# Kernel tuning notes

Hardware: AMD Instinct MI355X
Metric: run time of the kernel (lower is better)

The kernel has to match this reference:

```python
import jax, jax.numpy as jnp
import numpy as np

B, S, H = 2, 2048, 2048
HQ, HKV, DK, DV = 32, 8, 64, 64
G = HQ // HKV  # queries per kv group
SCALE = 1.0 / DK ** 0.5


def setup_inputs() -> dict:
    key = jax.random.key(0)
    k1, k2, k3, k4 = jax.random.split(key, 4)
    qkv_out = HQ * DK + HKV * (DK + DV)
    x = jax.random.normal(k1, (B, S, H), dtype=jnp.float32)
    Wqkv = jax.random.normal(k2, (H, qkv_out), dtype=jnp.float32) * (1.0 / np.sqrt(H))
    Wout = jax.random.normal(k3, (HQ * DV, H), dtype=jnp.float32) * (1.0 / np.sqrt(HQ * DV))
    b_out = jax.random.normal(k4, (H,), dtype=jnp.float32) * 0.01
    # causal mask [B, 1, S, S]; mask==0 positions are disallowed
    mask = jnp.broadcast_to(jnp.tril(jnp.ones((S, S), dtype=jnp.int32)), (B, 1, S, S))
    return {"x": x, "Wqkv": Wqkv, "Wout": Wout, "b_out": b_out, "mask": mask}


def reference(x, Wqkv, Wout, b_out, mask):
    # fused QKV projection (bias=False)
    qkv = x @ Wqkv  # [B, S, HQ*DK + HKV*(DK+DV)]
    tq, tk = HQ * DK, HKV * DK
    Q = qkv[..., :tq].reshape(B, S, HKV, G, DK)          # [B,S,n,g,d]
    K = qkv[..., tq:tq + tk].reshape(B, S, HKV, DK)       # [B,S,n,d]
    V = qkv[..., tq + tk:].reshape(B, S, HKV, DV)         # [B,S,n,e]
    # scores: [B, n(kv heads), g(group), s(query), t(key)]
    scores = jnp.einsum('bsngd,btnd->bngst', Q, K) * SCALE
    # mask [B,1,S,S] -> broadcast over n,g as [B,1,1,S,S]
    m = mask[:, :, None, :, :]
    scores = jnp.where(m == 0, -jnp.inf, scores)
    probs = jax.nn.softmax(scores, axis=-1)  # dropout p=0 -> identity
    attn = jnp.einsum('bngst,btne->bsnge', probs, V)      # [B,S,n,g,e]
    out = attn.reshape(B, S, HQ * DV) @ Wout + b_out       # [B,S,H]
    return out
```

## Files before the change

### kernel.cpp

```cpp
#include <hip/hip_runtime.h>

#define SEQ    2048
#define HDIM   2048
#define QKV_LD 3072
#define K_BASE 2048
#define V_BASE 2560
#define ATT_SCALE 0.125f
#define SM_MAX 20.0f
#define QK_MUL 0.18033688f
#define ZINIT  -28.8539008f

typedef __bf16 bf16x8 __attribute__((ext_vector_type(8)));
typedef float  f32x4  __attribute__((ext_vector_type(4)));
typedef float  f32x16 __attribute__((ext_vector_type(16)));
typedef unsigned short u16x8 __attribute__((ext_vector_type(8)));
typedef unsigned       u32x4 __attribute__((ext_vector_type(4)));

__device__ __forceinline__ void async_copy16(void* lds, const void* g) {
  __builtin_amdgcn_global_load_lds(
      (const __attribute__((address_space(1))) unsigned*)g,
      (__attribute__((address_space(3))) unsigned*)lds, 16, 0, 0);
}

__device__ __forceinline__ unsigned cvtpk(float lo, float hi) {
  unsigned r;
  asm("v_cvt_pk_bf16_f32 %0, %1, %2" : "=v"(r) : "v"(lo), "v"(hi));
  return r;
}
__device__ __forceinline__ void pl32swap(unsigned& a, unsigned& b) {
  asm("v_permlane32_swap_b32 %0, %1" : "+v"(a), "+v"(b));
}

__global__ void detect_dtype(const unsigned* __restrict__ p0,
                             const unsigned* __restrict__ p1,
                             const unsigned* __restrict__ p2,
                             const unsigned* __restrict__ p3,
                             int* __restrict__ flags) {
  const unsigned* ptrs[4] = {p0, p1, p2, p3};
  const int lane = threadIdx.x;
#pragma unroll
  for (int i = 0; i < 4; ++i) {
    int cnt = 0;
#pragma unroll
    for (int j = 0; j < 8; ++j) {
      unsigned w = ptrs[i][lane * 8 + j];
      unsigned e = (w >> 7) & 0xFF;
      cnt += (e >= 90 && e <= 160) ? 1 : 0;
    }
    for (int off = 32; off; off >>= 1) cnt += __shfl_down(cnt, off);
    if (lane == 0) flags[i] = (cnt < 350) ? 1 : 0;
  }
  if (lane == 0) flags[4] = 0;
}

__global__ __launch_bounds__(256) void cast_f32_bf16(const float* __restrict__ s,
                                                     __bf16* __restrict__ d) {
  const size_t i = ((size_t)blockIdx.x * 256 + threadIdx.x) * 8;
  float4 a = *(const float4*)(s + i);
  float4 b = *(const float4*)(s + i + 4);
  bf16x8 o;
  o[0] = (__bf16)a.x; o[1] = (__bf16)a.y; o[2] = (__bf16)a.z; o[3] = (__bf16)a.w;
  o[4] = (__bf16)b.x; o[5] = (__bf16)b.y; o[6] = (__bf16)b.z; o[7] = (__bf16)b.w;
  *(bf16x8*)(d + i) = o;
}

__global__ __launch_bounds__(256) void transpose_cast(const float* __restrict__ W,
                                                      __bf16* __restrict__ WT,
                                                      int K, int N) {
  __shared__ float T[64][68];
  const int tid = threadIdx.x;
  const int kb = blockIdx.y * 64, nb = blockIdx.x * 64;
  const int r = tid >> 2, cq = tid & 3;
  const float* src = W + (size_t)(kb + r) * N + nb + cq * 16;
  float4 f0 = ((const float4*)src)[0];
  float4 f1 = ((const float4*)src)[1];
  float4 f2 = ((const float4*)src)[2];
  float4 f3 = ((const float4*)src)[3];
  *(float4*)&T[r][cq * 16 + 0]  = f0;
  *(float4*)&T[r][cq * 16 + 4]  = f1;
  *(float4*)&T[r][cq * 16 + 8]  = f2;
  *(float4*)&T[r][cq * 16 + 12] = f3;
  __syncthreads();
  __bf16* dst = WT + (size_t)(nb + r) * K + kb + cq * 16;
  bf16x8 o0, o1;
#pragma unroll
  for (int j = 0; j < 8; ++j) o0[j] = (__bf16)T[cq * 16 + j][r];
#pragma unroll
  for (int j = 0; j < 8; ++j) o1[j] = (__bf16)T[cq * 16 + 8 + j][r];
  *(bf16x8*)dst = o0;
  *(bf16x8*)(dst + 8) = o1;
}

#define GT_ELE (256 * 64)

template <typename OutT>
__global__ __launch_bounds__(512, 2) void gemm256(const __bf16* __restrict__ A,
                                                  const __bf16* __restrict__ Bt,
                                                  const float* __restrict__ bias,
                                                  OutT* __restrict__ C,
                                                  int M, int N, int K) {
  extern __shared__ __align__(16) __bf16 smem[];
  __bf16* Asm = smem;
  __bf16* Bsm = smem + 2 * GT_ELE;

  const int tid = threadIdx.x;
  const int w = tid >> 6, lane = tid & 63;
  const int lr = lane & 15, lg = lane >> 4;
  const int wm = w >> 2, wn = w & 3;
  const int m0 = blockIdx.y * 256, n0 = blockIdx.x * 256;
  const int KT = K >> 6;

  const int lrow = lane >> 3;
  const int lc8  = ((lane & 7) ^ lrow) * 8;

  f32x4 acc[2][4][2][2];
#pragma unroll
  for (int a = 0; a < 2; ++a)
#pragma unroll
    for (int b = 0; b < 4; ++b)
#pragma unroll
      for (int c = 0; c < 2; ++c)
#pragma unroll
        for (int d = 0; d < 2; ++d) acc[a][b][c][d] = (f32x4){0.f, 0.f, 0.f, 0.f};

  bf16x8 af[4][2], bf[2][2];

  const __bf16* gA = A + (size_t)m0 * K;
  const __bf16* gB = Bt + (size_t)n0 * K;

  auto stA = [&](int h, int t) {
    __bf16* base = Asm + (size_t)(t & 1) * GT_ELE + (h * 128 + 16 * w) * 64;
    const __bf16* s = gA + (size_t)(h * 128 + 16 * w + lrow) * K + (size_t)t * 64 + lc8;
    async_copy16(base, s);
    async_copy16(base + 8 * 64, s + (size_t)8 * K);
  };
  auto stB = [&](int h, int t) {
    __bf16* base = Bsm + (size_t)(t & 1) * GT_ELE + (h * 128 + 16 * w) * 64;
    const __bf16* s = gB + (size_t)(h * 128 + 16 * w + lrow) * K + (size_t)t * 64 + lc8;
    async_copy16(base, s);
    async_copy16(base + 8 * 64, s + (size_t)8 * K);
  };

#define LOAD_A(mq)                                                              \
  {                                                                             \
    _Pragma("unroll") for (int mf = 0; mf < 4; ++mf)                            \
        _Pragma("unroll") for (int kk = 0; kk < 2; ++kk)                        \
            af[mf][kk] = *(const bf16x8*)&Ac[((mq) * 128 + wm * 64 + mf * 16 +  \
                                             lr) * 64 +                         \
                                            (((kk * 4 + lg) ^ (lr & 7)) << 3)]; \
  }
#define LOAD_B(nq)                                                              \
  {                                                                             \
    _Pragma("unroll") for (int nf = 0; nf < 2; ++nf)                            \
        _Pragma("unroll") for (int kk = 0; kk < 2; ++kk)                        \
            bf[nf][kk] = *(const bf16x8*)&Bc[((nq) * 128 + wn * 32 + nf * 16 +  \
                                             lr) * 64 +                         \
                                            (((kk * 4 + lg) ^ (lr & 7)) << 3)]; \
  }
#define MFMA_Q(mq, nq)                                                          \
  {                                                                             \
    __builtin_amdgcn_s_setprio(1);                                              \
    _Pragma("unroll") for (int mf = 0; mf < 4; ++mf)                            \
        _Pragma("unroll") for (int nf = 0; nf < 2; ++nf)                        \
            _Pragma("unroll") for (int kk = 0; kk < 2; ++kk)                    \
                acc[mq][mf][nq][nf] = __builtin_amdgcn_mfma_f32_16x16x32_bf16(  \
                    af[mf][kk], bf[nf][kk], acc[mq][mf][nq][nf], 0, 0, 0);      \
    __builtin_amdgcn_s_setprio(0);                                              \
  }
#define WAIT_LGKM                                                               \
  asm volatile("s_waitcnt lgkmcnt(0)" ::: "memory");                            \
  __builtin_amdgcn_sched_barrier(0);

  stA(0, 0); stB(1, 0); stA(1, 0); stB(0, 0);
  stA(0, 1); stB(1, 1);

  for (int kt = 0; kt < KT; ++kt) {
    const __bf16* Ac = Asm + (size_t)(kt & 1) * GT_ELE;
    const __bf16* Bc = Bsm + (size_t)(kt & 1) * GT_ELE;
    const bool p1 = kt + 1 < KT, p2 = kt + 2 < KT;

    if (p1) stA(1, kt + 1);
    if (p1) asm volatile("s_waitcnt vmcnt(6)" ::: "memory");
    else    asm volatile("s_waitcnt vmcnt(0)" ::: "memory");
    __builtin_amdgcn_s_barrier();
    LOAD_A(0); LOAD_B(0);
    WAIT_LGKM; MFMA_Q(0, 0);
    __builtin_amdgcn_s_barrier();

    LOAD_B(1);
    if (p1) stB(0, kt + 1);
    __builtin_amdgcn_s_barrier();
    WAIT_LGKM; MFMA_Q(0, 1);
    __builtin_amdgcn_s_barrier();

    LOAD_A(1);
    if (p2) stA(0, kt + 2);
    __builtin_amdgcn_s_barrier();
    WAIT_LGKM; MFMA_Q(1, 1);
    __builtin_amdgcn_s_barrier();

    LOAD_B(0);
    if (p2) stB(1, kt + 2);
    __builtin_amdgcn_s_barrier();
    WAIT_LGKM; MFMA_Q(1, 0);
    __builtin_amdgcn_s_barrier();
  }

#pragma unroll
  for (int mq = 0; mq < 2; ++mq)
#pragma unroll
    for (int mf = 0; mf < 4; ++mf)
#pragma unroll
      for (int nq = 0; nq < 2; ++nq)
#pragma unroll
        for (int nf = 0; nf < 2; ++nf)
#pragma unroll
          for (int r = 0; r < 4; ++r) {
            int row = m0 + mq * 128 + wm * 64 + mf * 16 + 4 * lg + r;
            int col = n0 + nq * 128 + wn * 32 + nf * 16 + lr;
            float v = acc[mq][mf][nq][nf][r];
            if (bias) v += bias[col];
            C[(size_t)row * N + col] = (OutT)v;
          }
#undef LOAD_A
#undef LOAD_B
#undef MFMA_Q
#undef WAIT_LGKM
}

#define GA_ELE (256 * 64)
#define GB_ELE (128 * 64)

template <typename OutT>
__global__ __launch_bounds__(512, 2) void gemm256x128(const __bf16* __restrict__ A,
                                                      const __bf16* __restrict__ Bt,
                                                      const float* __restrict__ bias,
                                                      OutT* __restrict__ C,
                                                      int M, int N, int K) {
  extern __shared__ __align__(16) __bf16 smem[];
  __bf16* Asm = smem;
  __bf16* Bsm = smem + 2 * GA_ELE;

  const int tid = threadIdx.x;
  const int w = tid >> 6, lane = tid & 63;
  const int lr = lane & 15, lg = lane >> 4;
  const int wm = w >> 2, wn = w & 3;
  const int m0 = blockIdx.y * 256, n0 = blockIdx.x * 128;
  const int KT = K >> 6;

  const int lrow = lane >> 3;
  const int lc8  = ((lane & 7) ^ lrow) * 8;

  f32x4 acc[2][4][2];
#pragma unroll
  for (int a = 0; a < 2; ++a)
#pragma unroll
    for (int b = 0; b < 4; ++b)
#pragma unroll
      for (int c = 0; c < 2; ++c) acc[a][b][c] = (f32x4){0.f, 0.f, 0.f, 0.f};

  bf16x8 af[4][2], bf[2][2];

  const __bf16* gA = A + (size_t)m0 * K;
  const __bf16* gB = Bt + (size_t)n0 * K;

  auto stA = [&](int h, int t) {
    __bf16* base = Asm + (size_t)(t & 1) * GA_ELE + (h * 128 + 16 * w) * 64;
    const __bf16* s = gA + (size_t)(h * 128 + 16 * w + lrow) * K + (size_t)t * 64 + lc8;
    async_copy16(base, s);
    async_copy16(base + 8 * 64, s + (size_t)8 * K);
  };
  auto stB = [&](int t) {
    __bf16* base = Bsm + (size_t)(t & 1) * GB_ELE + (16 * w) * 64;
    const __bf16* s = gB + (size_t)(16 * w + lrow) * K + (size_t)t * 64 + lc8;
    async_copy16(base, s);
    async_copy16(base + 8 * 64, s + (size_t)8 * K);
  };

#define LOAD_A(mq)                                                              \
  {                                                                             \
    _Pragma("unroll") for (int mf = 0; mf < 4; ++mf)                            \
        _Pragma("unroll") for (int kk = 0; kk < 2; ++kk)                        \
            af[mf][kk] = *(const bf16x8*)&Ac[((mq) * 128 + wm * 64 + mf * 16 +  \
                                             lr) * 64 +                         \
                                            (((kk * 4 + lg) ^ (lr & 7)) << 3)]; \
  }
#define LOAD_B                                                                  \
  {                                                                             \
    _Pragma("unroll") for (int nf = 0; nf < 2; ++nf)                            \
        _Pragma("unroll") for (int kk = 0; kk < 2; ++kk)                        \
            bf[nf][kk] = *(const bf16x8*)&Bc[(wn * 32 + nf * 16 + lr) * 64 +    \
                                            (((kk * 4 + lg) ^ (lr & 7)) << 3)]; \
  }
#define MFMA_Q(mq)                                                              \
  {                                                                             \
    __builtin_amdgcn_s_setprio(1);                                              \
    _Pragma("unroll") for (int mf = 0; mf < 4; ++mf)                            \
        _Pragma("unroll") for (int nf = 0; nf < 2; ++nf)                        \
            _Pragma("unroll") for (int kk = 0; kk < 2; ++kk)                    \
                acc[mq][mf][nf] = __builtin_amdgcn_mfma_f32_16x16x32_bf16(      \
                    af[mf][kk], bf[nf][kk], acc[mq][mf][nf], 0, 0, 0);          \
    __builtin_amdgcn_s_setprio(0);                                              \
  }
#define WAIT_LGKM                                                               \
  asm volatile("s_waitcnt lgkmcnt(0)" ::: "memory");                            \
  __builtin_amdgcn_sched_barrier(0);

  stA(0, 0); stB(0); stA(1, 0);
  stA(0, 1); stB(1);

  for (int kt = 0; kt < KT; ++kt) {
    const __bf16* Ac = Asm + (size_t)(kt & 1) * GA_ELE;
    const __bf16* Bc = Bsm + (size_t)(kt & 1) * GB_ELE;
    const bool p1 = kt + 1 < KT, p2 = kt + 2 < KT;

    if (p1) stA(1, kt + 1);
    if (p1) asm volatile("s_waitcnt vmcnt(6)" ::: "memory");
    else    asm volatile("s_waitcnt vmcnt(0)" ::: "memory");
    __builtin_amdgcn_s_barrier();
    LOAD_A(0); LOAD_B;
    WAIT_LGKM; MFMA_Q(0);
    __builtin_amdgcn_s_barrier();

    LOAD_A(1);
    if (p2) { stA(0, kt + 2); stB(kt + 2); }
    __builtin_amdgcn_s_barrier();
    WAIT_LGKM; MFMA_Q(1);
    __builtin_amdgcn_s_barrier();
  }

#pragma unroll
  for (int mq = 0; mq < 2; ++mq)
#pragma unroll
    for (int mf = 0; mf < 4; ++mf)
#pragma unroll
      for (int nf = 0; nf < 2; ++nf)
#pragma unroll
        for (int r = 0; r < 4; ++r) {
          int row = m0 + mq * 128 + wm * 64 + mf * 16 + 4 * lg + r;
          int col = n0 + wn * 32 + nf * 16 + lr;
          float v = acc[mq][mf][nf][r];
          if (bias) v += bias[col];
          C[(size_t)row * N + col] = (OutT)v;
        }
#undef LOAD_A
#undef LOAD_B
#undef MFMA_Q
#undef WAIT_LGKM
}

template <typename OutT>
__global__ __launch_bounds__(256) void gemm128(const __bf16* __restrict__ A,
                                               const __bf16* __restrict__ Bt,
                                               const float* __restrict__ bias,
                                               OutT* __restrict__ C,
                                               int M, int N, int K) {
  __shared__ __bf16 As[128 * 32];
  __shared__ __bf16 Bs[128 * 32];
  const int tid = threadIdx.x;
  const int w = tid >> 6, lane = tid & 63;
  const int lr = lane & 15, lg = lane >> 4;
  const int wm = w >> 1, wn = w & 1;
  const int m0 = blockIdx.y * 128, n0 = blockIdx.x * 128;

  f32x4 acc[4][4];
#pragma unroll
  for (int i = 0; i < 4; ++i)
#pragma unroll
    for (int j = 0; j < 4; ++j) acc[i][j] = (f32x4){0.f, 0.f, 0.f, 0.f};

  const int srow = 32 * w + (lane >> 2);
  const int scol = (lane & 3) * 8;
  const __bf16* ga = A + (size_t)(m0 + srow) * K + scol;
  const __bf16* gb = Bt + (size_t)(n0 + srow) * K + scol;
  __bf16* la0 = &As[(32 * w) * 32];
  __bf16* la1 = &As[(32 * w + 16) * 32];
  __bf16* lb0 = &Bs[(32 * w) * 32];
  __bf16* lb1 = &Bs[(32 * w + 16) * 32];

  for (int k0 = 0; k0 < K; k0 += 32) {
    async_copy16(la0, ga + k0);
    async_copy16(la1, ga + (size_t)16 * K + k0);
    async_copy16(lb0, gb + k0);
    async_copy16(lb1, gb + (size_t)16 * K + k0);
    __syncthreads();
    bf16x8 af[4], bfr[4];
#pragma unroll
    for (int mf = 0; mf < 4; ++mf)
      af[mf] = *(const bf16x8*)&As[(64 * wm + 16 * mf + lr) * 32 + 8 * lg];
#pragma unroll
    for (int nf = 0; nf < 4; ++nf)
      bfr[nf] = *(const bf16x8*)&Bs[(64 * wn + 16 * nf + lr) * 32 + 8 * lg];
#pragma unroll
    for (int mf = 0; mf < 4; ++mf)
#pragma unroll
      for (int nf = 0; nf < 4; ++nf)
        acc[mf][nf] = __builtin_amdgcn_mfma_f32_16x16x32_bf16(af[mf], bfr[nf],
                                                              acc[mf][nf], 0, 0, 0);
    __syncthreads();
  }

#pragma unroll
  for (int mf = 0; mf < 4; ++mf)
#pragma unroll
    for (int nf = 0; nf < 4; ++nf)
#pragma unroll
      for (int r = 0; r < 4; ++r) {
        int row = m0 + 64 * wm + 16 * mf + 4 * lg + r;
        int col = n0 + 64 * wn + 16 * nf + lr;
        float v = acc[mf][nf][r];
        if (bias) v += bias[col];
        C[(size_t)row * N + col] = (OutT)v;
      }
}

template <typename OutT>
__global__ __launch_bounds__(256) void gemm64(const void* __restrict__ Araw,
                                              const void* __restrict__ Braw,
                                              const void* __restrict__ biasraw,
                                              const int* __restrict__ flags,
                                              int fa, int fb, int fbias,
                                              OutT* __restrict__ C,
                                              int M, int N, int K) {
  __shared__ __bf16 As[64][40];
  __shared__ __bf16 Bs[64][40];
  const bool a_f32 = flags[fa] != 0;
  const bool b_f32 = flags[fb] != 0;
  const bool c_f32 = flags[fbias] != 0;
  const int tid = threadIdx.x;
  const int wave = tid >> 6, lane = tid & 63;
  const int lr = lane & 15, lg = lane >> 4;
  const int m0 = blockIdx.y * 64, n0 = blockIdx.x * 64;
  f32x4 acc[4];
#pragma unroll
  for (int i = 0; i < 4; ++i) acc[i] = (f32x4){0.f, 0.f, 0.f, 0.f};
  const int ar = tid >> 2, ac = (tid & 3) * 8;
  const int bn = tid & 63, bk0 = (tid >> 6) * 8;
  for (int k0 = 0; k0 < K; k0 += 32) {
    bf16x8 av;
    if (a_f32) {
      const float* p = (const float*)Araw + (size_t)(m0 + ar) * K + (k0 + ac);
#pragma unroll
      for (int j = 0; j < 8; ++j) av[j] = (__bf16)p[j];
    } else {
      av = *(const bf16x8*)((const __bf16*)Araw + (size_t)(m0 + ar) * K + (k0 + ac));
    }
    *(bf16x8*)&As[ar][ac] = av;
    if (b_f32) {
      const float* p = (const float*)Braw + (size_t)(k0 + bk0) * N + (n0 + bn);
#pragma unroll
      for (int j = 0; j < 8; ++j) Bs[bn][bk0 + j] = (__bf16)p[(size_t)j * N];
    } else {
      const __bf16* p = (const __bf16*)Braw + (size_t)(k0 + bk0) * N + (n0 + bn);
#pragma unroll
      for (int j = 0; j < 8; ++j) Bs[bn][bk0 + j] = p[(size_t)j * N];
    }
    __syncthreads();
    bf16x8 a = *(const bf16x8*)&As[wave * 16 + lr][lg * 8];
#pragma unroll
    for (int nt = 0; nt < 4; ++nt) {
      bf16x8 b = *(const bf16x8*)&Bs[nt * 16 + lr][lg * 8];
      acc[nt] = __builtin_amdgcn_mfma_f32_16x16x32_bf16(a, b, acc[nt], 0, 0, 0);
    }
    __syncthreads();
  }
#pragma unroll
  for (int nt = 0; nt < 4; ++nt)
#pragma unroll
    for (int r = 0; r < 4; ++r) {
      int row = m0 + wave * 16 + lg * 4 + r;
      int col = n0 + nt * 16 + lr;
      float v = acc[nt][r];
      if (biasraw) {
        v += c_f32 ? ((const float*)biasraw)[col]
                   : (float)((const __bf16*)biasraw)[col];
      }
      C[(size_t)row * N + col] = (OutT)v;
    }
}

__global__ __launch_bounds__(256) void attn_fused4(const __bf16* __restrict__ qkv,
                                                   __bf16* __restrict__ attn_out) {
  __shared__ __bf16 Ks[2][64][64];
  __shared__ __bf16 Vt[2][64][72];

  const int tid  = threadIdx.x;
  const int w    = tid >> 6;
  const int lane = tid & 63;
  const int lam  = lane & 31;
  const int hsel = lane >> 5;
  const int h8   = hsel * 8;

  const int bid = blockIdx.x;
  const int xcd = bid & 7;
  const int idx = bid >> 3;
  const int bh  = xcd * 2 + (idx >> 5);
  const int p   = idx & 31;
  const int hkv = bh & 7;
  const int b   = bh >> 3;
  const int h   = hkv * 4 + w;

  const int qclo = p, qchi = 63 - p;
  const int qlo0 = qclo * 32, qhi0 = qchi * 32;
  const int nlo = (qclo >> 1) + 1;
  const int nhi = (qchi >> 1) + 1;
  const int qglo = qlo0 + lam, qghi = qhi0 + lam;

  const size_t k_ch = K_BASE + (size_t)hkv * 64;
  const size_t v_ch = V_BASE + (size_t)hkv * 64;
  const __bf16* base = qkv + (size_t)b * SEQ * QKV_LD;

  bf16x8 aqlo[4], aqhi[4];
  {
    const __bf16* qrl = base + (size_t)(qlo0 + lam) * QKV_LD + (size_t)h * 64;
    const __bf16* qrh = base + (size_t)(qhi0 + lam) * QKV_LD + (size_t)h * 64;
#pragma unroll
    for (int c = 0; c < 4; ++c) {
      bf16x8 vl = *(const bf16x8*)(qrl + 16 * c + h8);
      bf16x8 vh = *(const bf16x8*)(qrh + 16 * c + h8);
#pragma unroll
      for (int j = 0; j < 8; ++j) {
        vl[j] = (__bf16)((float)vl[j] * QK_MUL);
        vh[j] = (__bf16)((float)vh[j] * QK_MUL);
      }
      aqlo[c] = vl;
      aqhi[c] = vh;
    }
  }

  bf16x8 bone;
#pragma unroll
  for (int j = 0; j < 8; ++j) bone[j] = (__bf16)1.0f;

  f32x16 o0l, o1l, oll, o0h, o1h, olh;
#pragma unroll
  for (int i = 0; i < 16; ++i) {
    o0l[i] = 0.f; o1l[i] = 0.f; oll[i] = 0.f;
    o0h[i] = 0.f; o1h[i] = 0.f; olh[i] = 0.f;
  }

  const int krow  = 16 * w + (lane >> 3);
  const int ksoct = ((lane & 7) ^ (lane >> 3)) * 8;
  const __bf16* kga = base + k_ch + (size_t)krow * QKV_LD + ksoct;
  const __bf16* kgb = kga + (size_t)8 * QKV_LD;
  const int kp = lane >> 3, cq = lane & 7;
  const __bf16* vg0 = base + v_ch + (size_t)(16 * w + 2 * kp) * QKV_LD + 8 * cq;
  const int vtcol = (((2 * w + (kp >> 2)) ^ cq) << 3) + 2 * (kp & 3);
  const int vtrow = 8 * cq;

  async_copy16(&Ks[0][16 * w][0],     kga);
  async_copy16(&Ks[0][16 * w + 8][0], kgb);
  bf16x8 va = *(const bf16x8*)vg0;
  bf16x8 vb = *(const bf16x8*)(vg0 + QKV_LD);
  {
    u16x8 ua = *(u16x8*)&va, ub = *(u16x8*)&vb;
#pragma unroll
    for (int j = 0; j < 8; ++j)
      *(unsigned*)&Vt[0][vtrow + j][vtcol] =
          (unsigned)ua[j] | ((unsigned)ub[j] << 16);
  }
  __syncthreads();

#define CHUNK_COMPUTE(AQ, O0, O1, OL, QG, KHMAX, KMASK)                        \
  {                                                                            \
    bf16x8 pa[4];                                                              \
    _Pragma("unroll") for (int kh = 0; kh < 2; ++kh) {                         \
      if (kh < (KHMAX)) {                                                      \
        f32x16 z;                                                              \
        _Pragma("unroll") for (int i = 0; i < 16; ++i) z[i] = ZINIT;           \
        __builtin_amdgcn_s_setprio(1);                                         \
        _Pragma("unroll") for (int c = 0; c < 4; ++c) {                        \
          bf16x8 kf = *(const bf16x8*)                                         \
              &Ks[cur][32 * kh + lam][(((2 * c + hsel) ^ (lam & 7)) << 3)];    \
          z = __builtin_amdgcn_mfma_f32_32x32x16_bf16(kf, AQ[c], z, 0, 0, 0);  \
        }                                                                      \
        __builtin_amdgcn_s_setprio(0);                                         \
        if (kh == (KMASK)) {                                                   \
          _Pragma("unroll") for (int i = 0; i < 16; ++i) {                     \
            const int t = t0 + 32 * kh + ((i & 3) + 8 * (i >> 2)) + 4 * hsel;  \
            float pp = __builtin_amdgcn_exp2f(z[i]);                           \
            z[i] = (t > (QG)) ? 0.f : pp;                                      \
          }                                                                    \
        } else {                                                               \
          _Pragma("unroll") for (int i = 0; i < 16; ++i)                       \
            z[i] = __builtin_amdgcn_exp2f(z[i]);                               \
        }                                                                      \
        unsigned c0 = cvtpk(z[0], z[1]),   c1 = cvtpk(z[2], z[3]);             \
        unsigned c2 = cvtpk(z[4], z[5]),   c3 = cvtpk(z[6], z[7]);             \
        unsigned c4 = cvtpk(z[8], z[9]),   c5 = cvtpk(z[10], z[11]);           \
        unsigned c6 = cvtpk(z[12], z[13]), c7 = cvtpk(z[14], z[15]);           \
        pl32swap(c0, c2); pl32swap(c1, c3);                                    \
        pl32swap(c4, c6); pl32swap(c5, c7);                                    \
        u32x4 pw0 = {c0, c1, c2, c3}, pw1 = {c4, c5, c6, c7};                  \
        pa[2 * kh]     = *(bf16x8*)&pw0;                                       \
        pa[2 * kh + 1] = *(bf16x8*)&pw1;                                       \
      }                                                                        \
    }                                                                          \
    const int ksmax = (KHMAX) * 2;                                             \
    __builtin_amdgcn_s_setprio(1);                                             \
    _Pragma("unroll") for (int ks = 0; ks < 4; ++ks) {                         \
      if (ks < ksmax) {                                                        \
        OL = __builtin_amdgcn_mfma_f32_32x32x16_bf16(pa[ks], bone, OL, 0,0,0); \
        {                                                                      \
          bf16x8 bv = *(const bf16x8*)                                         \
              &Vt[cur][lam][(((2 * ks + hsel) ^ ((lam >> 3) & 7)) << 3)];      \
          O0 = __builtin_amdgcn_mfma_f32_32x32x16_bf16(pa[ks], bv, O0, 0,0,0); \
        }                                                                      \
        {                                                                      \
          const int e = 32 + lam;                                              \
          bf16x8 bv = *(const bf16x8*)                                         \
              &Vt[cur][e][(((2 * ks + hsel) ^ ((e >> 3) & 7)) << 3)];          \
          O1 = __builtin_amdgcn_mfma_f32_32x32x16_bf16(pa[ks], bv, O1, 0,0,0); \
        }                                                                      \
      }                                                                        \
    }                                                                          \
    __builtin_amdgcn_s_setprio(0);                                             \
  }

  for (int blk = 0; blk < nhi; ++blk) {
    const int cur  = blk & 1;
    const int t0   = blk * 64;
    const bool havenext = (blk + 1 < nhi);

    if (havenext) {
      const __bf16* vg = vg0 + (size_t)(t0 + 64) * QKV_LD;
      va = *(const bf16x8*)vg;
      vb = *(const bf16x8*)(vg + QKV_LD);
      const size_t koff = (size_t)(t0 + 64) * QKV_LD;
      async_copy16(&Ks[cur ^ 1][16 * w][0],     kga + koff);
      async_copy16(&Ks[cur ^ 1][16 * w + 8][0], kgb + koff);
    }

    {
      const bool diag = (blk == nhi - 1);
      const int khmax = (diag && !(qchi & 1)) ? 1 : 2;
      const int kmask = diag ? ((qchi & 1) ? 1 : 0) : 2;
      CHUNK_COMPUTE(aqhi, o0h, o1h, olh, qghi, khmax, kmask);
    }
    if (blk < nlo) {
      const bool diag = (blk == nlo - 1);
      const int khmax = (diag && !(qclo & 1)) ? 1 : 2;
      const int kmask = diag ? ((qclo & 1) ? 1 : 0) : 2;
      CHUNK_COMPUTE(aqlo, o0l, o1l, oll, qglo, khmax, kmask);
    }

    if (havenext) {
      u16x8 ua = *(u16x8*)&va, ub = *(u16x8*)&vb;
#pragma unroll
      for (int j = 0; j < 8; ++j)
        *(unsigned*)&Vt[cur ^ 1][vtrow + j][vtcol] =
            (unsigned)ua[j] | ((unsigned)ub[j] << 16);
    }
    __syncthreads();
  }
#undef CHUNK_COMPUTE

#define CHUNK_OUT(O0, O1, OL, Q0)                                              \
  {                                                                            \
    float inv[16];                                                             \
    _Pragma("unroll") for (int i = 0; i < 16; ++i) inv[i] = 1.0f / OL[i];      \
    __bf16* dst = attn_out + ((size_t)b * SEQ + (Q0)) * HDIM +                 \
                  (size_t)h * 64 + lam;                                        \
    _Pragma("unroll") for (int i = 0; i < 16; ++i) {                           \
      const int rq = (i & 3) + 8 * (i >> 2) + 4 * hsel;                        \
      dst[(size_t)rq * HDIM]      = (__bf16)(O0[i] * inv[i]);                  \
      dst[(size_t)rq * HDIM + 32] = (__bf16)(O1[i] * inv[i]);                  \
    }                                                                          \
  }

  CHUNK_OUT(o0h, o1h, olh, qhi0);
  CHUNK_OUT(o0l, o1l, oll, qlo0);
#undef CHUNK_OUT
}

extern "C" void kernel_launch(void* const* d_in, const int* in_sizes, int n_in,
                              void* d_out, int out_size, void* d_ws, size_t ws_size,
                              hipStream_t stream) {
  const void* x     = d_in[0];
  const void* Wqkv  = d_in[1];
  const void* Wout  = d_in[2];
  const void* b_out = d_in[3];
  float* out = (float*)d_out;

  const int M = 2 * SEQ;
  __bf16* qkv  = (__bf16*)d_ws;
  __bf16* attn = qkv + (size_t)M * QKV_LD;
  int* flags   = (int*)(attn + (size_t)M * HDIM);
  __bf16* xb   = (__bf16*)((char*)flags + 64);
  __bf16* wqt  = xb + (size_t)M * HDIM;
  __bf16* wot  = wqt + (size_t)QKV_LD * HDIM;

  const size_t need = (size_t)((char*)(wot + (size_t)HDIM * HDIM) - (char*)d_ws);

  static int dyn_ok = -1;
  if (dyn_ok < 0) {
    hipError_t e1 = hipFuncSetAttribute(
        reinterpret_cast<const void*>(&gemm256<__bf16>),
        hipFuncAttributeMaxDynamicSharedMemorySize, 131072);
    hipError_t e2 = hipFuncSetAttribute(
        reinterpret_cast<const void*>(&gemm256x128<float>),
        hipFuncAttributeMaxDynamicSharedMemorySize, 98304);
    dyn_ok = (e1 == hipSuccess && e2 == hipSuccess) ? 1 : 0;
  }

  detect_dtype<<<1, 64, 0, stream>>>((const unsigned*)x, (const unsigned*)Wqkv,
                                     (const unsigned*)Wout, (const unsigned*)b_out,
                                     flags);

  if (ws_size >= need) {
    cast_f32_bf16<<<dim3((M * HDIM) / 2048), 256, 0, stream>>>((const float*)x, xb);
    transpose_cast<<<dim3(QKV_LD / 64, HDIM / 64), 256, 0, stream>>>(
        (const float*)Wqkv, wqt, HDIM, QKV_LD);
    transpose_cast<<<dim3(HDIM / 64, HDIM / 64), 256, 0, stream>>>(
        (const float*)Wout, wot, HDIM, HDIM);

    if (dyn_ok) {
      gemm256<__bf16><<<dim3(QKV_LD / 256, M / 256), 512, 131072, stream>>>(
          xb, wqt, nullptr, qkv, M, QKV_LD, HDIM);
      attn_fused4<<<dim3(512), 256, 0, stream>>>(qkv, attn);
      gemm256x128<float><<<dim3(HDIM / 128, M / 256), 512, 98304, stream>>>(
          attn, wot, (const float*)b_out, out, M, HDIM, HDIM);
    } else {
      gemm128<__bf16><<<dim3(QKV_LD / 128, M / 128), 256, 0, stream>>>(
          xb, wqt, nullptr, qkv, M, QKV_LD, HDIM);
      attn_fused4<<<dim3(512), 256, 0, stream>>>(qkv, attn);
      gemm128<float><<<dim3(HDIM / 128, M / 128), 256, 0, stream>>>(
          attn, wot, (const float*)b_out, out, M, HDIM, HDIM);
    }
  } else {
    gemm64<__bf16><<<dim3(QKV_LD / 64, M / 64), 256, 0, stream>>>(
        x, Wqkv, nullptr, flags, 0, 1, 3, qkv, M, QKV_LD, HDIM);
    attn_fused4<<<dim3(512), 256, 0, stream>>>(qkv, attn);
    gemm64<float><<<dim3(HDIM / 64, M / 64), 256, 0, stream>>>(
        attn, Wout, b_out, flags, 4, 2, 3, out, M, HDIM, HDIM);
  }
}
```

Before: 303.9 us.

## Replace 256x256 QKV GEMM with 128x192 tiles and grouped block swizzle

The QKV projection GEMM moves from 256x256 tiles (96 blocks) to 128x192 tiles launched as a 1D grid of 512 blocks with an XCD-aware swizzle. This gives more blocks than the 256 CUs, fills the machine better and shrinks LDS use so more blocks can be resident per CU (launch bounds 4). The pipeline is rebuilt with two MFMA phases per k-step instead of four. In exchange, each tile reuses less data per load and the arithmetic intensity per block drops.

```diff
diff --git a/kernel.cpp b/kernel.cpp
--- a/kernel.cpp
+++ b/kernel.cpp
@@ -91,141 +91,128 @@
   *(bf16x8*)(dst + 8) = o1;
 }
 
-#define GT_ELE (256 * 64)
+#define QA_ELE (128 * 64)
+#define QB_ELE (192 * 64)
 
 template <typename OutT>
-__global__ __launch_bounds__(512, 2) void gemm256(const __bf16* __restrict__ A,
-                                                  const __bf16* __restrict__ Bt,
-                                                  const float* __restrict__ bias,
-                                                  OutT* __restrict__ C,
-                                                  int M, int N, int K) {
+__global__ __launch_bounds__(512, 4) void gemm128x192(const __bf16* __restrict__ A,
+                                                      const __bf16* __restrict__ Bt,
+                                                      const float* __restrict__ bias,
+                                                      OutT* __restrict__ C,
+                                                      int M, int N, int K) {
   extern __shared__ __align__(16) __bf16 smem[];
   __bf16* Asm = smem;
-  __bf16* Bsm = smem + 2 * GT_ELE;
+  __bf16* Bsm = smem + 2 * QA_ELE;
 
   const int tid = threadIdx.x;
   const int w = tid >> 6, lane = tid & 63;
   const int lr = lane & 15, lg = lane >> 4;
   const int wm = w >> 2, wn = w & 3;
-  const int m0 = blockIdx.y * 256, n0 = blockIdx.x * 256;
+  const int bid = blockIdx.x;
+  const int cpx = gridDim.x >> 3;
+  const int swz = (bid & 7) * cpx + (bid >> 3);
+  const int nx = N / 192;
+  const int m0 = (swz / nx) * 128, n0 = (swz % nx) * 192;
   const int KT = K >> 6;
 
   const int lrow = lane >> 3;
   const int lc8  = ((lane & 7) ^ lrow) * 8;
 
-  f32x4 acc[2][4][2][2];
-#pragma unroll
-  for (int a = 0; a < 2; ++a)
-#pragma unroll
-    for (int b = 0; b < 4; ++b)
-#pragma unroll
-      for (int c = 0; c < 2; ++c)
-#pragma unroll
-        for (int d = 0; d < 2; ++d) acc[a][b][c][d] = (f32x4){0.f, 0.f, 0.f, 0.f};
-
-  bf16x8 af[4][2], bf[2][2];
+  f32x4 acc[4][3];
+#pragma unroll
+  for (int a = 0; a < 4; ++a)
+#pragma unroll
+    for (int b = 0; b < 3; ++b) acc[a][b] = (f32x4){0.f, 0.f, 0.f, 0.f};
+
+  bf16x8 af[4][2], bf[3][2];
 
   const __bf16* gA = A + (size_t)m0 * K;
   const __bf16* gB = Bt + (size_t)n0 * K;
 
-  auto stA = [&](int h, int t) {
-    __bf16* base = Asm + (size_t)(t & 1) * GT_ELE + (h * 128 + 16 * w) * 64;
-    const __bf16* s = gA + (size_t)(h * 128 + 16 * w + lrow) * K + (size_t)t * 64 + lc8;
+  auto stA = [&](int t) {
+    __bf16* base = Asm + (size_t)(t & 1) * QA_ELE + (16 * w) * 64;
+    const __bf16* s = gA + (size_t)(16 * w + lrow) * K + (size_t)t * 64 + lc8;
     async_copy16(base, s);
     async_copy16(base + 8 * 64, s + (size_t)8 * K);
   };
-  auto stB = [&](int h, int t) {
-    __bf16* base = Bsm + (size_t)(t & 1) * GT_ELE + (h * 128 + 16 * w) * 64;
-    const __bf16* s = gB + (size_t)(h * 128 + 16 * w + lrow) * K + (size_t)t * 64 + lc8;
+  auto stB01 = [&](int t) {
+    __bf16* base = Bsm + (size_t)(t & 1) * QB_ELE + (8 * w) * 64;
+    const __bf16* s = gB + (size_t)(8 * w + lrow) * K + (size_t)t * 64 + lc8;
     async_copy16(base, s);
-    async_copy16(base + 8 * 64, s + (size_t)8 * K);
+    async_copy16(base + 64 * 64, s + (size_t)64 * K);
   };
-
-#define LOAD_A(mq)                                                              \
+  auto stB2 = [&](int t) {
+    __bf16* base = Bsm + (size_t)(t & 1) * QB_ELE + (128 + 8 * w) * 64;
+    const __bf16* s = gB + (size_t)(128 + 8 * w + lrow) * K + (size_t)t * 64 + lc8;
+    async_copy16(base, s);
+  };
+
+#define QLOAD_A                                                                 \
   {                                                                             \
     _Pragma("unroll") for (int mf = 0; mf < 4; ++mf)                            \
         _Pragma("unroll") for (int kk = 0; kk < 2; ++kk)                        \
-            af[mf][kk] = *(const bf16x8*)&Ac[((mq) * 128 + wm * 64 + mf * 16 +  \
-                                             lr) * 64 +                         \
+            af[mf][kk] = *(const bf16x8*)&Ac[(wm * 64 + mf * 16 + lr) * 64 +    \
                                             (((kk * 4 + lg) ^ (lr & 7)) << 3)]; \
   }
-#define LOAD_B(nq)                                                              \
+#define QLOAD_B(nf)                                                             \
   {                                                                             \
-    _Pragma("unroll") for (int nf = 0; nf < 2; ++nf)                            \
-        _Pragma("unroll") for (int kk = 0; kk < 2; ++kk)                        \
-            bf[nf][kk] = *(const bf16x8*)&Bc[((nq) * 128 + wn * 32 + nf * 16 +  \
-                                             lr) * 64 +                         \
-                                            (((kk * 4 + lg) ^ (lr & 7)) << 3)]; \
-  }
-#define MFMA_Q(mq, nq)                                                          \
+    _Pragma("unroll") for (int kk = 0; kk < 2; ++kk)                            \
+        bf[nf][kk] = *(const bf16x8*)&Bc[(wn * 48 + (nf) * 16 + lr) * 64 +      \
+                                        (((kk * 4 + lg) ^ (lr & 7)) << 3)];     \
+  }
+#define QMFMA(nfs, nfe)                                                         \
   {                                                                             \
     __builtin_amdgcn_s_setprio(1);                                              \
     _Pragma("unroll") for (int mf = 0; mf < 4; ++mf)                            \
-        _Pragma("unroll") for (int nf = 0; nf < 2; ++nf)                        \
+        _Pragma("unroll") for (int nf = (nfs); nf < (nfe); ++nf)                \
             _Pragma("unroll") for (int kk = 0; kk < 2; ++kk)                    \
-                acc[mq][mf][nq][nf] = __builtin_amdgcn_mfma_f32_16x16x32_bf16(  \
-                    af[mf][kk], bf[nf][kk], acc[mq][mf][nq][nf], 0, 0, 0);      \
+                acc[mf][nf] = __builtin_amdgcn_mfma_f32_16x16x32_bf16(          \
+                    af[mf][kk], bf[nf][kk], acc[mf][nf], 0, 0, 0);              \
     __builtin_amdgcn_s_setprio(0);                                              \
   }
-#define WAIT_LGKM                                                               \
+#define QWAIT_LGKM                                                              \
   asm volatile("s_waitcnt lgkmcnt(0)" ::: "memory");                            \
   __builtin_amdgcn_sched_barrier(0);
 
-  stA(0, 0); stB(1, 0); stA(1, 0); stB(0, 0);
-  stA(0, 1); stB(1, 1);
+  stA(0); stB01(0); stB2(0);
+  stA(1); stB01(1);
 
   for (int kt = 0; kt < KT; ++kt) {
-    const __bf16* Ac = Asm + (size_t)(kt & 1) * GT_ELE;
-    const __bf16* Bc = Bsm + (size_t)(kt & 1) * GT_ELE;
+    const __bf16* Ac = Asm + (size_t)(kt & 1) * QA_ELE;
+    const __bf16* Bc = Bsm + (size_t)(kt & 1) * QB_ELE;
     const bool p1 = kt + 1 < KT, p2 = kt + 2 < KT;
 
-    if (p1) stA(1, kt + 1);
-    if (p1) asm volatile("s_waitcnt vmcnt(6)" ::: "memory");
+    if (p1) stB2(kt + 1);
+    if (p1) asm volatile("s_waitcnt vmcnt(5)" ::: "memory");
     else    asm volatile("s_waitcnt vmcnt(0)" ::: "memory");
     __builtin_amdgcn_s_barrier();
-    LOAD_A(0); LOAD_B(0);
-    WAIT_LGKM; MFMA_Q(0, 0);
+    QLOAD_A; QLOAD_B(0); QLOAD_B(1);
+    QWAIT_LGKM; QMFMA(0, 2);
     __builtin_amdgcn_s_barrier();
 
-    LOAD_B(1);
-    if (p1) stB(0, kt + 1);
+    QLOAD_B(2);
+    if (p2) { stA(kt + 2); stB01(kt + 2); }
     __builtin_amdgcn_s_barrier();
-    WAIT_LGKM; MFMA_Q(0, 1);
+    QWAIT_LGKM; QMFMA(2, 3);
     __builtin_amdgcn_s_barrier();
-
-    LOAD_A(1);
-    if (p2) stA(0, kt + 2);
-    __builtin_amdgcn_s_barrier();
-    WAIT_LGKM; MFMA_Q(1, 1);
-    __builtin_amdgcn_s_barrier();
-
-    LOAD_B(0);
-    if (p2) stB(1, kt + 2);
-    __builtin_amdgcn_s_barrier();
-    WAIT_LGKM; MFMA_Q(1, 0);
-    __builtin_amdgcn_s_barrier();
-  }
-
-#pragma unroll
-  for (int mq = 0; mq < 2; ++mq)
-#pragma unroll
-    for (int mf = 0; mf < 4; ++mf)
-#pragma unroll
-      for (int nq = 0; nq < 2; ++nq)
-#pragma unroll
-        for (int nf = 0; nf < 2; ++nf)
-#pragma unroll
-          for (int r = 0; r < 4; ++r) {
-            int row = m0 + mq * 128 + wm * 64 + mf * 16 + 4 * lg + r;
-            int col = n0 + nq * 128 + wn * 32 + nf * 16 + lr;
-            float v = acc[mq][mf][nq][nf][r];
-            if (bias) v += bias[col];
-            C[(size_t)row * N + col] = (OutT)v;
-          }
-#undef LOAD_A
-#undef LOAD_B
-#undef MFMA_Q
-#undef WAIT_LGKM
+  }
+
+#pragma unroll
+  for (int mf = 0; mf < 4; ++mf)
+#pragma unroll
+    for (int nf = 0; nf < 3; ++nf)
+#pragma unroll
+      for (int r = 0; r < 4; ++r) {
+        int row = m0 + wm * 64 + mf * 16 + 4 * lg + r;
+        int col = n0 + wn * 48 + nf * 16 + lr;
+        float v = acc[mf][nf][r];
+        if (bias) v += bias[col];
+        C[(size_t)row * N + col] = (OutT)v;
+      }
+#undef QLOAD_A
+#undef QLOAD_B
+#undef QMFMA
+#undef QWAIT_LGKM
 }
 
 #define GA_ELE (256 * 64)
@@ -695,8 +682,8 @@
   static int dyn_ok = -1;
   if (dyn_ok < 0) {
     hipError_t e1 = hipFuncSetAttribute(
-        reinterpret_cast<const void*>(&gemm256<__bf16>),
-        hipFuncAttributeMaxDynamicSharedMemorySize, 131072);
+        reinterpret_cast<const void*>(&gemm128x192<__bf16>),
+        hipFuncAttributeMaxDynamicSharedMemorySize, 81920);
     hipError_t e2 = hipFuncSetAttribute(
         reinterpret_cast<const void*>(&gemm256x128<float>),
         hipFuncAttributeMaxDynamicSharedMemorySize, 98304);
@@ -715,7 +702,7 @@
         (const float*)Wout, wot, HDIM, HDIM);
 
     if (dyn_ok) {
-      gemm256<__bf16><<<dim3(QKV_LD / 256, M / 256), 512, 131072, stream>>>(
+      gemm128x192<__bf16><<<dim3(512), 512, 81920, stream>>>(
           xb, wqt, nullptr, qkv, M, QKV_LD, HDIM);
       attn_fused4<<<dim3(512), 256, 0, stream>>>(qkv, attn);
       gemm256x128<float><<<dim3(HDIM / 128, M / 256), 512, 98304, stream>>>(
```

Measured after the change: 305.1 us. Within noise of the previous version (+0.4%).
